# Optimization experiments

Hardware: AMD Instinct MI355X
Metric: run time of the kernel (lower is better)

Reference implementation:

```python
import jax, jax.numpy as jnp
import numpy as np

EPS = 1e-5

def layer_norm(x, gamma):
    mu = jnp.mean(x, axis=-1, keepdims=True)
    var = jnp.mean(jnp.square(x - mu), axis=-1, keepdims=True)
    return (x - mu) / jnp.sqrt(var + EPS) * gamma

def setup_inputs() -> dict:
    key = jax.random.key(0)
    ks = jax.random.split(key, 10)
    b, n, j = 2, 2048, 2048
    dim, ctx_dim, heads, dim_head, ff_mult = 1024, 1024, 16, 64, 4
    inner = heads * dim_head
    ff_inner = ff_mult * dim
    s = 0.02
    return {
        'x': jax.random.normal(ks[0], (b, n, dim), jnp.float32),
        'context': jax.random.normal(ks[1], (b, j, ctx_dim), jnp.float32),
        'mask': jax.random.randint(ks[2], (b, j), 0, 2, jnp.int32),
        'gamma': jnp.ones((dim,), jnp.float32),
        'ctx_gamma': jnp.ones((ctx_dim,), jnp.float32),
        'Wq': jax.random.normal(ks[3], (dim, inner), jnp.float32) * s,
        'Wkv': jax.random.normal(ks[4], (ctx_dim, 2 * dim_head), jnp.float32) * s,
        'Wout': jax.random.normal(ks[5], (inner, dim), jnp.float32) * s,
        'Wff1': jax.random.normal(ks[6], (dim, 2 * ff_inner), jnp.float32) * s,
        'Wff2': jax.random.normal(ks[7], (ff_inner, dim), jnp.float32) * s,
    }

def reference(x, context, mask, gamma, ctx_gamma, Wq, Wkv, Wout, Wff1, Wff2):
    heads, dim_head = 16, 64
    b, n, dim = x.shape
    scale = dim_head ** -0.5
    xn = layer_norm(x, gamma)                              # [b,n,dim]
    ctx = layer_norm(context, ctx_gamma)                   # [b,j,cd]
    q = (xn @ Wq).reshape(b, n, heads, dim_head).transpose(0, 2, 1, 3) * scale  # [b,h,n,d]
    kv = ctx @ Wkv                                         # [b,j,2d]
    k, v = kv[..., :dim_head], kv[..., dim_head:]          # [b,j,d] each (multi-query)
    sim = jnp.einsum('bhid,bjd->bhij', q, k)               # [b,h,n,j]
    sim = jnp.where((mask == 0)[:, None, None, :], -jnp.inf, sim)
    attn = jax.nn.softmax(sim, axis=-1)
    out = jnp.einsum('bhij,bjd->bhid', attn, v)            # [b,h,n,d]
    out = out.transpose(0, 2, 1, 3).reshape(b, n, heads * dim_head)
    out = out @ Wout                                       # [b,n,dim]
    # parallel SwiGLU FF on normalized x
    h = xn @ Wff1
    ff_inner = Wff2.shape[0]
    a, gate = h[..., :ff_inner], h[..., ff_inner:]
    out = out + (jax.nn.silu(gate) * a) @ Wff2
    return out
```

## Files before the change

kernel.cpp:

```cpp
#include <hip/hip_runtime.h>

typedef unsigned short u16;
typedef unsigned int   u32;
typedef __bf16  bf16x8 __attribute__((ext_vector_type(8)));
typedef __bf16  bf16x2 __attribute__((ext_vector_type(2)));
typedef float   f32x4  __attribute__((ext_vector_type(4)));

static __device__ __forceinline__ float b2f(u16 v) {
    return __builtin_bit_cast(float, (u32)(((u32)v) << 16));
}
static __device__ __forceinline__ u16 f2b(float f) {
    u32 u = __builtin_bit_cast(u32, f);
    return (u16)((u + 0x7FFFu + ((u >> 16) & 1u)) >> 16);
}
static __device__ __forceinline__ u32 pack2(float a, float b) {
    bf16x2 t; t[0] = (__bf16)a; t[1] = (__bf16)b;
    return __builtin_bit_cast(u32, t);
}

__global__ __launch_bounds__(256)
void ln_kernel(const float* __restrict__ x, const float* __restrict__ ctx,
               const float* __restrict__ gamma, const float* __restrict__ cgamma,
               u16* __restrict__ xn, u16* __restrict__ ctxn)
{
    const int row = blockIdx.x;
    const int tid = threadIdx.x;
    const float* src; const float* g; u16* dst;
    if (row < 4096) { src = x   + (long)row * 1024;          g = gamma;  dst = xn   + (long)row * 1024; }
    else            { src = ctx + (long)(row - 4096) * 1024; g = cgamma; dst = ctxn + (long)(row - 4096) * 1024; }
    float4 v = ((const float4*)src)[tid];
    float s = v.x + v.y + v.z + v.w;
    float q = v.x*v.x + v.y*v.y + v.z*v.z + v.w*v.w;
#pragma unroll
    for (int off = 32; off; off >>= 1) { s += __shfl_xor(s, off); q += __shfl_xor(q, off); }
    __shared__ float r1[4], r2[4];
    if ((tid & 63) == 0) { r1[tid >> 6] = s; r2[tid >> 6] = q; }
    __syncthreads();
    s = r1[0] + r1[1] + r1[2] + r1[3];
    q = r2[0] + r2[1] + r2[2] + r2[3];
    float mu   = s * (1.0f / 1024.0f);
    float var  = q * (1.0f / 1024.0f) - mu * mu;
    float rstd = rsqrtf(var + 1e-5f);
    float4 gv = ((const float4*)g)[tid];
    ushort4 o;
    o.x = f2b((v.x - mu) * rstd * gv.x);
    o.y = f2b((v.y - mu) * rstd * gv.y);
    o.z = f2b((v.z - mu) * rstd * gv.z);
    o.w = f2b((v.w - mu) * rstd * gv.w);
    ((ushort4*)dst)[tid] = o;
}

__global__ __launch_bounds__(256)
void wconv(const float* __restrict__ W, u16* __restrict__ Wt, int N, int K, float scale)
{
    __shared__ float tile[32][33];
    const int tid = threadIdx.x;
    const int n0 = blockIdx.x * 32;
    const int k0 = blockIdx.y * 32;
    const int r  = tid >> 3;
    const int c4 = (tid & 7) * 4;
    float4 v = *(const float4*)&W[(long)(k0 + r) * N + n0 + c4];
    tile[r][c4 + 0] = v.x; tile[r][c4 + 1] = v.y; tile[r][c4 + 2] = v.z; tile[r][c4 + 3] = v.w;
    __syncthreads();
    ushort4 o;
    o.x = f2b(tile[c4 + 0][r] * scale);
    o.y = f2b(tile[c4 + 1][r] * scale);
    o.z = f2b(tile[c4 + 2][r] * scale);
    o.w = f2b(tile[c4 + 3][r] * scale);
    *(ushort4*)&Wt[(long)(n0 + r) * K + k0 + c4] = o;
}

__global__ __launch_bounds__(256)
void wconv_ff1(const float* __restrict__ W, u16* __restrict__ Wt)
{
    __shared__ float tile[32][33];
    const int tid = threadIdx.x;
    const int a  = blockIdx.x;
    const int k0 = blockIdx.y * 32;
    const int r  = tid >> 3;
    const int c4 = (tid & 7) * 4;
    const int srccol = (c4 < 16) ? (a * 16 + c4) : (4096 + a * 16 + (c4 - 16));
    float4 v = *(const float4*)&W[(long)(k0 + r) * 8192 + srccol];
    tile[r][c4 + 0] = v.x; tile[r][c4 + 1] = v.y; tile[r][c4 + 2] = v.z; tile[r][c4 + 3] = v.w;
    __syncthreads();
    ushort4 o;
    o.x = f2b(tile[c4 + 0][r]);
    o.y = f2b(tile[c4 + 1][r]);
    o.z = f2b(tile[c4 + 2][r]);
    o.w = f2b(tile[c4 + 3][r]);
    *(ushort4*)&Wt[(long)(a * 32 + r) * 1024 + k0 + c4] = o;
}

__global__ __launch_bounds__(256)
void kext_build(const float* __restrict__ kvf, const int* __restrict__ mask,
                u16* __restrict__ kext, float* __restrict__ mbias)
{
    const int gid = blockIdx.x * 256 + threadIdx.x;
    const int b = gid >> 14;
    const int rem = gid & 16383;
    const int j = rem >> 3;
    const int c = rem & 7;
    const float* src = &kvf[((long)b * 2048 + j) * 128 + c * 8];
    u16 ov[8];
#pragma unroll
    for (int e = 0; e < 8; ++e) ov[e] = f2b(src[e]);
    uint4 w;
    w.x = (u32)ov[0] | ((u32)ov[1] << 16);
    w.y = (u32)ov[2] | ((u32)ov[3] << 16);
    w.z = (u32)ov[4] | ((u32)ov[5] << 16);
    w.w = (u32)ov[6] | ((u32)ov[7] << 16);
    *(uint4*)&kext[((long)b * 2048 + j) * 64 + c * 8] = w;
    if (c == 0) mbias[b * 2048 + j] = mask[b * 2048 + j] ? 0.0f : -1e30f;
}

__global__ __launch_bounds__(256)
void vtrans(const float* __restrict__ kvf, u16* __restrict__ vT)
{
    const int j = blockIdx.x * 256 + threadIdx.x;
    const int d = blockIdx.y;
    const int b = blockIdx.z;
    vT[(long)b * 64 * 2048 + (long)d * 2048 + j] =
        f2b(kvf[((long)b * 2048 + j) * 128 + 64 + d]);
}

#define BM 128
#define BN 128
#define BK 32

template<int EPI>
__global__ __launch_bounds__(256, 2)
void gemm_bt(const u16* __restrict__ A, const u16* __restrict__ Bt,
             void* __restrict__ Cv,
             int K, int lda, int ldb, int ldc,
             long aH, long bH, long cH)
{
    __shared__ __align__(16) u16 sm[2][2][BM * BK];
    const int tid  = threadIdx.x;
    const int wave = tid >> 6;
    const int lane = tid & 63;
    const int tn = blockIdx.x * BN;
    const int tm = blockIdx.y * BM;
    const int z  = blockIdx.z;
    A  += (long)z * aH;
    Bt += (long)z * bH;

    const int arow0 = (tid >> 2);
    const int arow1 = 64 + (tid >> 2);
    const int acs0  = (tid & 3) ^ ((arow0 >> 1) & 3);
    const int acs1  = (tid & 3) ^ ((arow1 >> 1) & 3);
    const int nt = K / BK;

#define STAGE(buf, k0)                                                                              \
    do {                                                                                            \
        __builtin_amdgcn_global_load_lds(                                                           \
            (const __attribute__((address_space(1))) void*)(A + (long)(tm + arow0) * lda + (k0) + acs0 * 8),   \
            (__attribute__((address_space(3))) void*)(&sm[buf][0][(wave * 64) * 8]), 16, 0, 0);     \
        __builtin_amdgcn_global_load_lds(                                                           \
            (const __attribute__((address_space(1))) void*)(A + (long)(tm + arow1) * lda + (k0) + acs1 * 8),   \
            (__attribute__((address_space(3))) void*)(&sm[buf][0][(256 + wave * 64) * 8]), 16, 0, 0); \
        __builtin_amdgcn_global_load_lds(                                                           \
            (const __attribute__((address_space(1))) void*)(Bt + (long)(tn + arow0) * ldb + (k0) + acs0 * 8),  \
            (__attribute__((address_space(3))) void*)(&sm[buf][1][(wave * 64) * 8]), 16, 0, 0);     \
        __builtin_amdgcn_global_load_lds(                                                           \
            (const __attribute__((address_space(1))) void*)(Bt + (long)(tn + arow1) * ldb + (k0) + acs1 * 8),  \
            (__attribute__((address_space(3))) void*)(&sm[buf][1][(256 + wave * 64) * 8]), 16, 0, 0); \
    } while (0)

    STAGE(0, 0);

    f32x4 acc[4][4] = {};
    const int wr   = (wave >> 1) * 64;
    const int wc   = (wave & 1) * 64;
    const int frow = lane & 15;
    const int fk   = lane >> 4;

    for (int t = 0; t < nt; ++t) {
        __syncthreads();
        if (t + 1 < nt) STAGE((t + 1) & 1, (t + 1) * BK);
        const int cur = t & 1;
        bf16x8 af[4], bf[4];
#pragma unroll
        for (int m = 0; m < 4; ++m) {
            int row = wr + m * 16 + frow;
            af[m] = *(const bf16x8*)&sm[cur][0][row * BK + ((fk ^ ((row >> 1) & 3)) * 8)];
        }
#pragma unroll
        for (int n = 0; n < 4; ++n) {
            int row = wc + n * 16 + frow;
            bf[n] = *(const bf16x8*)&sm[cur][1][row * BK + ((fk ^ ((row >> 1) & 3)) * 8)];
        }
#pragma unroll
        for (int m = 0; m < 4; ++m)
#pragma unroll
            for (int n = 0; n < 4; ++n)
                acc[m][n] = __builtin_amdgcn_mfma_f32_16x16x32_bf16(af[m], bf[n], acc[m][n], 0, 0, 0);
    }
#undef STAGE

    const long coff = (long)z * cH;
#pragma unroll
    for (int m = 0; m < 4; ++m) {
        const int row0 = tm + wr + m * 16 + fk * 4;
#pragma unroll
        for (int n = 0; n < 4; ++n) {
            const int col = tn + wc + n * 16 + frow;
#pragma unroll
            for (int r = 0; r < 4; ++r) {
                const long off = coff + (long)(row0 + r) * ldc + col;
                const float v = acc[m][n][r];
                if constexpr (EPI == 0)      ((u16*)Cv)[off] = f2b(v);
                else if constexpr (EPI == 1) ((float*)Cv)[off] = v;
                else if constexpr (EPI == 2) ((float*)Cv)[off] += v;
                else                         atomicAdd(&((float*)Cv)[off], v);
            }
        }
    }
}

__global__ __launch_bounds__(512, 2)
void gemm256_ff1(const u16* __restrict__ A, const u16* __restrict__ Bt,
                 u16* __restrict__ C, int K, int lda, int ldb, int ldc)
{
    __shared__ __align__(16) u16 As[2][256 * 64];
    __shared__ __align__(16) u16 Bs[2][256 * 64];
    const int tid  = threadIdx.x;
    const int wave = tid >> 6, lane = tid & 63;
    const int wm = wave >> 2, wn = wave & 3;
    const int frow = lane & 15, fk = lane >> 4;
    const int tn = blockIdx.x * 256;
    const int tm = blockIdx.y * 256;
    const int nt = K >> 6;

    int arow[4], acs[4];
#pragma unroll
    for (int i = 0; i < 4; ++i) {
        const int slot = i * 512 + tid;
        arow[i] = slot >> 3;
        acs[i]  = ((slot & 7) ^ (arow[i] & 7)) * 8;
    }

#define STAGE256(buf, k0)                                                                            \
    do {                                                                                             \
        _Pragma("unroll")                                                                            \
        for (int i = 0; i < 4; ++i) {                                                                \
            __builtin_amdgcn_global_load_lds(                                                        \
                (const __attribute__((address_space(1))) void*)(A + (long)(tm + arow[i]) * lda + (k0) + acs[i]),  \
                (__attribute__((address_space(3))) void*)(&As[buf][(i * 512 + wave * 64) * 8]), 16, 0, 0);        \
            __builtin_amdgcn_global_load_lds(                                                        \
                (const __attribute__((address_space(1))) void*)(Bt + (long)(tn + arow[i]) * ldb + (k0) + acs[i]), \
                (__attribute__((address_space(3))) void*)(&Bs[buf][(i * 512 + wave * 64) * 8]), 16, 0, 0);        \
        }                                                                                            \
    } while (0)

    STAGE256(0, 0);
    STAGE256(1, 64);
    asm volatile("s_waitcnt vmcnt(8)" ::: "memory");
    __builtin_amdgcn_sched_barrier(0);
    __builtin_amdgcn_s_barrier();

    f32x4 acc[8][4] = {};

    for (int t = 0; ; ++t) {
        const int cur = t & 1;
        const u16* as = &As[cur][0];
        const u16* bs = &Bs[cur][0];
#pragma unroll
        for (int kk = 0; kk < 2; ++kk) {
            bf16x8 af[8], bfr[4];
#pragma unroll
            for (int mf = 0; mf < 8; ++mf) {
                const int row = wm * 128 + mf * 16 + frow;
                af[mf] = *(const bf16x8*)&as[row * 64 + (((kk * 4 + fk) ^ (row & 7)) * 8)];
            }
#pragma unroll
            for (int nf = 0; nf < 4; ++nf) {
                const int row = wn * 64 + nf * 16 + frow;
                bfr[nf] = *(const bf16x8*)&bs[row * 64 + (((kk * 4 + fk) ^ (row & 7)) * 8)];
            }
            __builtin_amdgcn_s_setprio(1);
#pragma unroll
            for (int mf = 0; mf < 8; ++mf)
#pragma unroll
                for (int nf = 0; nf < 4; ++nf)
                    acc[mf][nf] = __builtin_amdgcn_mfma_f32_16x16x32_bf16(af[mf], bfr[nf], acc[mf][nf], 0, 0, 0);
            __builtin_amdgcn_s_setprio(0);
        }
        if (t == nt - 1) break;
        __builtin_amdgcn_sched_barrier(0);
        __builtin_amdgcn_s_barrier();
        if (t + 2 < nt) {
            STAGE256(cur, (t + 2) << 6);
            asm volatile("s_waitcnt vmcnt(8)" ::: "memory");
        } else {
            asm volatile("s_waitcnt vmcnt(0)" ::: "memory");
        }
        __builtin_amdgcn_sched_barrier(0);
        __builtin_amdgcn_s_barrier();
    }
#undef STAGE256

#pragma unroll
    for (int mf = 0; mf < 8; ++mf) {
        const int gr = tm + wm * 128 + mf * 16 + fk * 4;
#pragma unroll
        for (int np = 0; np < 4; np += 2) {
            const int scol = (tn >> 1) + (wn * 2 + (np >> 1)) * 16 + frow;
            const f32x4 av = acc[mf][np];
            const f32x4 gv = acc[mf][np + 1];
#pragma unroll
            for (int r = 0; r < 4; ++r) {
                const float g = gv[r];
                const float o = av[r] * g / (1.0f + __expf(-g));
                C[(long)(gr + r) * ldc + scol] = f2b(o);
            }
        }
    }
}

__global__ __launch_bounds__(256, 4)
void flash_attn(const u16* __restrict__ qb, const u16* __restrict__ kext,
                const u16* __restrict__ vT, const float* __restrict__ mbias,
                u16* __restrict__ aout)
{
    __shared__ __align__(16) u16 Ksm[2][4096];
    __shared__ __align__(16) u16 Vsm[2][4096];
    __shared__ __align__(16) u16 Psm[4][1024];
    const int tid  = threadIdx.x;
    const int wave = tid >> 6, lane = tid & 63;
    const int frow = lane & 15, fk = lane >> 4;
    const int b = blockIdx.z, h = blockIdx.y;
    const int q0 = blockIdx.x * 64;

    const u16* kx = kext + (long)b * 2048 * 64;
    const u16* vb = vT   + (long)b * 64 * 2048;
    const float* mbb = mbias + b * 2048;

    const u16* qbase = qb + ((long)(b * 2048 + q0 + wave * 16 + frow)) * 1024 + h * 64;
    bf16x8 bq[2];
#pragma unroll
    for (int kk = 0; kk < 2; ++kk)
        bq[kk] = *(const bf16x8*)&qbase[kk * 32 + fk * 8];

#define FSTAGE(buf, j0s)                                                                             \
    do {                                                                                             \
        _Pragma("unroll")                                                                            \
        for (int i = 0; i < 2; ++i) {                                                                \
            const int slot = i * 256 + tid;                                                          \
            const int row  = slot >> 3;                                                              \
            const int csrc = (slot & 7) ^ (row & 7);                                                 \
            __builtin_amdgcn_global_load_lds(                                                        \
                (const __attribute__((address_space(1))) void*)(kx + (long)((j0s) + row) * 64 + csrc * 8), \
                (__attribute__((address_space(3))) void*)(&Ksm[buf][(i * 256 + wave * 64) * 8]), 16, 0, 0); \
            __builtin_amdgcn_global_load_lds(                                                        \
                (const __attribute__((address_space(1))) void*)(vb + (long)row * 2048 + (j0s) + csrc * 8),  \
                (__attribute__((address_space(3))) void*)(&Vsm[buf][(i * 256 + wave * 64) * 8]), 16, 0, 0); \
        }                                                                                            \
    } while (0)

    FSTAGE(0, 0);

    f32x4 oacc[4] = {};
    float mrun = -1e30f, lrun = 0.0f;
    u16* pw = &Psm[wave][0];

    for (int it = 0; it < 32; ++it) {
        const int j0 = it * 64;
        __syncthreads();
        float4 mb[4];
#pragma unroll
        for (int m = 0; m < 4; ++m)
            mb[m] = *(const float4*)&mbb[j0 + m * 16 + fk * 4];
        if (it + 1 < 32) FSTAGE((it + 1) & 1, (it + 1) * 64);
        const int cur = it & 1;

        f32x4 st[4] = {};
        __builtin_amdgcn_s_setprio(1);
#pragma unroll
        for (int kk = 0; kk < 2; ++kk) {
            bf16x8 ka[4];
#pragma unroll
            for (int m = 0; m < 4; ++m) {
                const int row = m * 16 + frow;
                ka[m] = *(const bf16x8*)&Ksm[cur][row * 64 + (((kk * 4 + fk) ^ (row & 7)) * 8)];
            }
#pragma unroll
            for (int m = 0; m < 4; ++m)
                st[m] = __builtin_amdgcn_mfma_f32_16x16x32_bf16(ka[m], bq[kk], st[m], 0, 0, 0);
        }
        __builtin_amdgcn_s_setprio(0);

        float sb[4][4];
#pragma unroll
        for (int m = 0; m < 4; ++m)
#pragma unroll
            for (int r = 0; r < 4; ++r) sb[m][r] = st[m][r] + (&mb[m].x)[r];
        float pm = fmaxf(
            fmaxf(fmaxf(sb[0][0], sb[0][1]), fmaxf(sb[0][2], sb[0][3])),
            fmaxf(fmaxf(sb[1][0], sb[1][1]), fmaxf(sb[1][2], sb[1][3])));
        pm = fmaxf(pm, fmaxf(
            fmaxf(fmaxf(sb[2][0], sb[2][1]), fmaxf(sb[2][2], sb[2][3])),
            fmaxf(fmaxf(sb[3][0], sb[3][1]), fmaxf(sb[3][2], sb[3][3]))));
        pm = fmaxf(pm, __shfl_xor(pm, 16));
        pm = fmaxf(pm, __shfl_xor(pm, 32));
        const float nm = fmaxf(mrun, pm);
        const float alpha = __expf(mrun - nm);
        mrun = nm;

        float rs = 0.0f;
#pragma unroll
        for (int m = 0; m < 4; ++m) {
            const float p0 = __expf(sb[m][0] - nm);
            const float p1 = __expf(sb[m][1] - nm);
            const float p2 = __expf(sb[m][2] - nm);
            const float p3 = __expf(sb[m][3] - nm);
            rs += (p0 + p1) + (p2 + p3);
            const int chunk = (m * 2 + (fk >> 1)) ^ (frow & 7);
            uint2 w; w.x = pack2(p0, p1); w.y = pack2(p2, p3);
            *(uint2*)&pw[frow * 64 + chunk * 8 + (fk & 1) * 4] = w;
        }
        rs += __shfl_xor(rs, 16);
        rs += __shfl_xor(rs, 32);
        lrun = lrun * alpha + rs;
#pragma unroll
        for (int mo = 0; mo < 4; ++mo)
#pragma unroll
            for (int r = 0; r < 4; ++r) oacc[mo][r] *= alpha;

        __builtin_amdgcn_s_setprio(1);
#pragma unroll
        for (int kkv = 0; kkv < 2; ++kkv) {
            bf16x8 va[4];
#pragma unroll
            for (int mo = 0; mo < 4; ++mo) {
                const int row = mo * 16 + frow;
                va[mo] = *(const bf16x8*)&Vsm[cur][row * 64 + (((kkv * 4 + fk) ^ (row & 7)) * 8)];
            }
            const bf16x8 pb = *(const bf16x8*)&pw[frow * 64 + (((kkv * 4 + fk) ^ (frow & 7)) * 8)];
#pragma unroll
            for (int mo = 0; mo < 4; ++mo)
                oacc[mo] = __builtin_amdgcn_mfma_f32_16x16x32_bf16(va[mo], pb, oacc[mo], 0, 0, 0);
        }
        __builtin_amdgcn_s_setprio(0);
    }
#undef FSTAGE

    const float inv = 1.0f / lrun;
    const long row = (long)b * 2048 + q0 + wave * 16 + frow;
#pragma unroll
    for (int mo = 0; mo < 4; ++mo) {
        uint2 w;
        w.x = pack2(oacc[mo][0] * inv, oacc[mo][1] * inv);
        w.y = pack2(oacc[mo][2] * inv, oacc[mo][3] * inv);
        *(uint2*)&aout[row * 1024 + h * 64 + mo * 16 + fk * 4] = w;
    }
}

extern "C" void kernel_launch(void* const* d_in, const int* in_sizes, int n_in,
                              void* d_out, int out_size, void* d_ws, size_t ws_size,
                              hipStream_t stream)
{
    const float* x      = (const float*)d_in[0];
    const float* ctx    = (const float*)d_in[1];
    const int*   mask   = (const int*)d_in[2];
    const float* gamma  = (const float*)d_in[3];
    const float* cgamma = (const float*)d_in[4];
    const float* Wq     = (const float*)d_in[5];
    const float* Wkv    = (const float*)d_in[6];
    const float* Wout   = (const float*)d_in[7];
    const float* Wff1   = (const float*)d_in[8];
    const float* Wff2   = (const float*)d_in[9];
    float* out = (float*)d_out;

    char* w = (char*)d_ws;
    auto carveB = [&](long bytes) { char* p = w; w += ((bytes + 255) / 256) * 256; return p; };
    u16*   xn     = (u16*)  carveB(4096L * 1024 * 2);
    u16*   ctxn   = (u16*)  carveB(4096L * 1024 * 2);
    u16*   WqT    = (u16*)  carveB(1024L * 1024 * 2);
    u16*   WkvT   = (u16*)  carveB(128L * 1024 * 2);
    u16*   WoutT  = (u16*)  carveB(1024L * 1024 * 2);
    u16*   Wff1Tp = (u16*)  carveB(8192L * 1024 * 2);
    u16*   Wff2T  = (u16*)  carveB(1024L * 4096 * 2);
    u16*   q      = (u16*)  carveB(4096L * 1024 * 2);
    float* kvf    = (float*)carveB(2L * 2048 * 128 * 4);
    u16*   kext   = (u16*)  carveB(2L * 2048 * 64 * 2);
    float* mbias  = (float*)carveB(2L * 2048 * 4);
    u16*   vT     = (u16*)  carveB(2L * 64 * 2048 * 2);
    u16*   aout   = (u16*)  carveB(4096L * 1024 * 2);
    u16*   gbuf   = (u16*)  carveB(4096L * 4096 * 2);

    dim3 B(256);

    ln_kernel<<<dim3(8192), B, 0, stream>>>(x, ctx, gamma, cgamma, xn, ctxn);
    wconv<<<dim3(32, 32),  B, 0, stream>>>(Wq,   WqT,   1024, 1024, 0.125f);
    wconv<<<dim3(4, 32),   B, 0, stream>>>(Wkv,  WkvT,  128,  1024, 1.0f);
    wconv<<<dim3(32, 32),  B, 0, stream>>>(Wout, WoutT, 1024, 1024, 1.0f);
    wconv_ff1<<<dim3(256, 32), B, 0, stream>>>(Wff1, Wff1Tp);
    wconv<<<dim3(32, 128), B, 0, stream>>>(Wff2, Wff2T, 1024, 4096, 1.0f);

    gemm_bt<0><<<dim3(8, 32, 1), B, 0, stream>>>(xn, WqT, q, 1024, 1024, 1024, 1024, 0, 0, 0);
    hipMemsetAsync(kvf, 0, 2L * 2048 * 128 * 4, stream);
    gemm_bt<4><<<dim3(1, 32, 4), B, 0, stream>>>(ctxn, WkvT, kvf, 256, 1024, 1024, 128, 256, 256, 0);
    kext_build<<<dim3(128), B, 0, stream>>>(kvf, mask, kext, mbias);
    vtrans<<<dim3(8, 64, 2), B, 0, stream>>>(kvf, vT);

    flash_attn<<<dim3(32, 16, 2), B, 0, stream>>>(q, kext, vT, mbias, aout);

    gemm_bt<1><<<dim3(8, 32, 1), B, 0, stream>>>(aout, WoutT, out, 1024, 1024, 1024, 1024, 0, 0, 0);
    gemm256_ff1<<<dim3(32, 16), dim3(512), 0, stream>>>(xn, Wff1Tp, gbuf, 1024, 1024, 1024, 4096);
    gemm_bt<2><<<dim3(8, 32, 1), B, 0, stream>>>(gbuf, Wff2T, out, 4096, 4096, 4096, 1024, 0, 0, 0);
}
```

Baseline: 417.1 us.

## Split FF1 GEMM main loop into four quadrant phases with interleaved staging; split-K FF2

The 256x256 FF1 GEMM now splits each K-tile into four phases, one per output quadrant. Each phase issues a quarter of the next tile's global-to-LDS loads while the MFMAs run, instead of staging whole tiles between barriers. This finer software pipeline is meant to hide load latency and spread memory traffic, at the cost of more barriers per tile. Separately, the FF2 GEMM switches to the gemm_bt<4> split-K variant with two K-splits. That doubles the grid to fill more CUs but relies on atomic accumulation into out, which already holds the Wout result.

```diff
diff --git a/kernel.cpp b/kernel.cpp
--- a/kernel.cpp
+++ b/kernel.cpp
@@ -231,73 +231,89 @@
     const int tm = blockIdx.y * 256;
     const int nt = K >> 6;
 
-    int arow[4], acs[4];
-#pragma unroll
-    for (int i = 0; i < 4; ++i) {
-        const int slot = i * 512 + tid;
-        arow[i] = slot >> 3;
-        acs[i]  = ((slot & 7) ^ (arow[i] & 7)) * 8;
-    }
-
-#define STAGE256(buf, k0)                                                                            \
-    do {                                                                                             \
-        _Pragma("unroll")                                                                            \
-        for (int i = 0; i < 4; ++i) {                                                                \
-            __builtin_amdgcn_global_load_lds(                                                        \
-                (const __attribute__((address_space(1))) void*)(A + (long)(tm + arow[i]) * lda + (k0) + acs[i]),  \
-                (__attribute__((address_space(3))) void*)(&As[buf][(i * 512 + wave * 64) * 8]), 16, 0, 0);        \
-            __builtin_amdgcn_global_load_lds(                                                        \
-                (const __attribute__((address_space(1))) void*)(Bt + (long)(tn + arow[i]) * ldb + (k0) + acs[i]), \
-                (__attribute__((address_space(3))) void*)(&Bs[buf][(i * 512 + wave * 64) * 8]), 16, 0, 0);        \
-        }                                                                                            \
-    } while (0)
-
-    STAGE256(0, 0);
-    STAGE256(1, 64);
-    asm volatile("s_waitcnt vmcnt(8)" ::: "memory");
+    const int lrow  = lane >> 3;
+    const int csrc8 = ((lane & 7) ^ lrow) * 8;
+    int rbA0[2], rbA1[2], rbB0[2], rbB1[2];
+#pragma unroll
+    for (int g = 0; g < 2; ++g) {
+        const int c = g * 8 + wave;
+        const int a0 = ((c >> 3) * 128) + ((c & 7) * 8);
+        rbA0[g] = a0; rbA1[g] = a0 + 64;
+        const int b0 = ((c >> 2) * 64) + ((c & 3) * 8);
+        rbB0[g] = b0; rbB1[g] = b0 + 32;
+    }
+
+#define STG(LDS, buf, src, toff, ld, kt, rb)                                                        \
+    __builtin_amdgcn_global_load_lds(                                                               \
+        (const __attribute__((address_space(1))) void*)((src) + (long)((toff) + (rb) + lrow) * (ld) + ((kt) << 6) + csrc8), \
+        (__attribute__((address_space(3))) void*)(&LDS[buf][(rb) * 64]), 16, 0, 0)
+
+#define STAGE_A0(buf, kt) do { STG(As, buf, A,  tm, lda, kt, rbA0[0]); STG(As, buf, A,  tm, lda, kt, rbA0[1]); } while (0)
+#define STAGE_A1(buf, kt) do { STG(As, buf, A,  tm, lda, kt, rbA1[0]); STG(As, buf, A,  tm, lda, kt, rbA1[1]); } while (0)
+#define STAGE_B0(buf, kt) do { STG(Bs, buf, Bt, tn, ldb, kt, rbB0[0]); STG(Bs, buf, Bt, tn, ldb, kt, rbB0[1]); } while (0)
+#define STAGE_B1(buf, kt) do { STG(Bs, buf, Bt, tn, ldb, kt, rbB1[0]); STG(Bs, buf, Bt, tn, ldb, kt, rbB1[1]); } while (0)
+
+    STAGE_B0(0, 0); STAGE_A0(0, 0); STAGE_A1(0, 0); STAGE_B1(0, 0);
+    if (nt > 1) {
+        STAGE_B0(1, 1); STAGE_A0(1, 1);
+        asm volatile("s_waitcnt vmcnt(4)" ::: "memory");
+    } else {
+        asm volatile("s_waitcnt vmcnt(0)" ::: "memory");
+    }
     __builtin_amdgcn_sched_barrier(0);
     __builtin_amdgcn_s_barrier();
 
     f32x4 acc[8][4] = {};
 
-    for (int t = 0; ; ++t) {
-        const int cur = t & 1;
-        const u16* as = &As[cur][0];
-        const u16* bs = &Bs[cur][0];
-#pragma unroll
-        for (int kk = 0; kk < 2; ++kk) {
-            bf16x8 af[8], bfr[4];
-#pragma unroll
-            for (int mf = 0; mf < 8; ++mf) {
-                const int row = wm * 128 + mf * 16 + frow;
-                af[mf] = *(const bf16x8*)&as[row * 64 + (((kk * 4 + fk) ^ (row & 7)) * 8)];
-            }
-#pragma unroll
-            for (int nf = 0; nf < 4; ++nf) {
-                const int row = wn * 64 + nf * 16 + frow;
-                bfr[nf] = *(const bf16x8*)&bs[row * 64 + (((kk * 4 + fk) ^ (row & 7)) * 8)];
-            }
-            __builtin_amdgcn_s_setprio(1);
-#pragma unroll
-            for (int mf = 0; mf < 8; ++mf)
-#pragma unroll
-                for (int nf = 0; nf < 4; ++nf)
-                    acc[mf][nf] = __builtin_amdgcn_mfma_f32_16x16x32_bf16(af[mf], bfr[nf], acc[mf][nf], 0, 0, 0);
-            __builtin_amdgcn_s_setprio(0);
-        }
-        if (t == nt - 1) break;
-        __builtin_amdgcn_sched_barrier(0);
+#define PHASE(mh, nh, STAGE_STMT)                                                                   \
+    {                                                                                               \
+        bf16x8 af[4][2], bfr[2][2];                                                                 \
+        _Pragma("unroll") for (int i = 0; i < 4; ++i) {                                             \
+            const int row = wm * 128 + (mh) * 64 + i * 16 + frow;                                   \
+            _Pragma("unroll") for (int kk = 0; kk < 2; ++kk)                                        \
+                af[i][kk] = *(const bf16x8*)&As[cur][row * 64 + (((kk * 4 + fk) ^ (row & 7)) * 8)]; \
+        }                                                                                           \
+        _Pragma("unroll") for (int j = 0; j < 2; ++j) {                                             \
+            const int row = wn * 64 + (nh) * 32 + j * 16 + frow;                                    \
+            _Pragma("unroll") for (int kk = 0; kk < 2; ++kk)                                        \
+                bfr[j][kk] = *(const bf16x8*)&Bs[cur][row * 64 + (((kk * 4 + fk) ^ (row & 7)) * 8)];\
+        }                                                                                           \
+        STAGE_STMT;                                                                                 \
+        __builtin_amdgcn_s_barrier();                                                               \
+        asm volatile("s_waitcnt lgkmcnt(0)" ::: "memory");                                          \
+        __builtin_amdgcn_sched_barrier(0);                                                          \
+        __builtin_amdgcn_s_setprio(1);                                                              \
+        _Pragma("unroll") for (int kk = 0; kk < 2; ++kk)                                            \
+            _Pragma("unroll") for (int i = 0; i < 4; ++i)                                           \
+                _Pragma("unroll") for (int j = 0; j < 2; ++j)                                       \
+                    acc[(mh) * 4 + i][(nh) * 2 + j] = __builtin_amdgcn_mfma_f32_16x16x32_bf16(      \
+                        af[i][kk], bfr[j][kk], acc[(mh) * 4 + i][(nh) * 2 + j], 0, 0, 0);           \
+        __builtin_amdgcn_s_setprio(0);                                                              \
+        __builtin_amdgcn_sched_barrier(0);                                                          \
+    }
+
+    for (int t = 0; t < nt; ++t) {
+        const int cur = t & 1, nxt = cur ^ 1;
+        PHASE(0, 0, if (t + 1 < nt) STAGE_A1(nxt, t + 1));
         __builtin_amdgcn_s_barrier();
-        if (t + 2 < nt) {
-            STAGE256(cur, (t + 2) << 6);
-            asm volatile("s_waitcnt vmcnt(8)" ::: "memory");
-        } else {
-            asm volatile("s_waitcnt vmcnt(0)" ::: "memory");
-        }
-        __builtin_amdgcn_sched_barrier(0);
+        PHASE(1, 0, if (t + 1 < nt) STAGE_B1(nxt, t + 1));
         __builtin_amdgcn_s_barrier();
-    }
-#undef STAGE256
+        PHASE(0, 1, if (t + 2 < nt) STAGE_B0(cur, t + 2));
+        __builtin_amdgcn_s_barrier();
+        PHASE(1, 1, if (t + 2 < nt) STAGE_A0(cur, t + 2));
+        if (t + 1 < nt) {
+            if (t + 2 < nt) asm volatile("s_waitcnt vmcnt(4)" ::: "memory");
+            else            asm volatile("s_waitcnt vmcnt(0)" ::: "memory");
+            __builtin_amdgcn_sched_barrier(0);
+            __builtin_amdgcn_s_barrier();
+        }
+    }
+#undef PHASE
+#undef STAGE_A0
+#undef STAGE_A1
+#undef STAGE_B0
+#undef STAGE_B1
+#undef STG
 
 #pragma unroll
     for (int mf = 0; mf < 8; ++mf) {
@@ -507,5 +523,5 @@
 
     gemm_bt<1><<<dim3(8, 32, 1), B, 0, stream>>>(aout, WoutT, out, 1024, 1024, 1024, 1024, 0, 0, 0);
     gemm256_ff1<<<dim3(32, 16), dim3(512), 0, stream>>>(xn, Wff1Tp, gbuf, 1024, 1024, 1024, 4096);
-    gemm_bt<2><<<dim3(8, 32, 1), B, 0, stream>>>(gbuf, Wff2T, out, 4096, 4096, 4096, 1024, 0, 0, 0);
-}
+    gemm_bt<4><<<dim3(8, 32, 2), B, 0, stream>>>(gbuf, Wff2T, out, 2048, 4096, 4096, 1024, 2048, 2048, 0);
+}
```

Measured after the change: 418.7 us. About the same (+0.4%).
